# Performance work log

Measured on AMD Instinct MI355X. Metric: run time of the kernel, lower is better.

The kernel has to match this reference:

```python
import jax, jax.numpy as jnp
import numpy as np

EPS = 1e-6
INV_T = 100.0
STEPS = 7  # eval_steps


def setup_inputs() -> dict:
    key = jax.random.key(0)
    k1, k2 = jax.random.split(key)
    B, C, H, W, R = 8, 512, 128, 128, 64
    x = jax.random.uniform(k1, (B, C, H, W), dtype=jnp.float32)
    bases = jax.random.uniform(k2, (B, C, R), dtype=jnp.float32)
    # _build_bases: F.normalize(bases, dim=1) -> L2 normalize over D
    bases = bases / jnp.maximum(jnp.linalg.norm(bases, axis=1, keepdims=True), 1e-12)
    return {"x": x, "bases": bases}


def _nmf(xf, bases):
    # xf: [B, D, N], bases: [B, D, R]
    # coef init: softmax(inv_t * x^T @ bases) over R
    coef = jax.nn.softmax(INV_T * jnp.einsum('bdn,bdr->bnr', xf, bases), axis=-1)

    def step(carry, _):
        bases, coef = carry
        # multiplicative update for coef: coef * (x^T B) / (coef (B^T B))
        num = jnp.einsum('bdn,bdr->bnr', xf, bases)          # [B,N,R]
        den = coef @ (jnp.swapaxes(bases, 1, 2) @ bases)      # [B,N,R]
        coef = coef * num / (den + EPS)
        # multiplicative update for bases: B * (x coef) / (B (coef^T coef))
        num = jnp.einsum('bdn,bnr->bdr', xf, coef)            # [B,D,R]
        den = bases @ (jnp.swapaxes(coef, 1, 2) @ coef)       # [B,D,R]
        bases = bases * num / (den + EPS)
        return (bases, coef), None

    (bases, coef), _ = jax.lax.scan(step, (bases, coef), None, length=STEPS)
    # compute_coef: one final coef update
    num = jnp.einsum('bdn,bdr->bnr', xf, bases)
    den = coef @ (jnp.swapaxes(bases, 1, 2) @ bases)
    coef = coef * num / (den + EPS)
    return bases, coef


def reference(x, bases):
    B, C, H, W = x.shape
    N = H * W
    xf = x.reshape(B, C, N)  # S=1, D=C
    bases, coef = _nmf(xf, bases)
    out = jnp.einsum('bdr,bnr->bdn', bases, coef)  # bases @ coef^T
    return out.reshape(B, C, H, W)
```

## Files before the change

### kernel.cpp

```cpp
#include <hip/hip_runtime.h>
#include <cstdint>
#include <cstddef>

namespace {

constexpr int B_ = 8;
constexpr int D_ = 512;
constexpr int N_ = 16384;
constexpr int R_ = 64;
constexpr float EPS_ = 1e-6f;
constexpr float INVT_ = 100.0f;

typedef __attribute__((ext_vector_type(4))) float f32x4;
typedef __attribute__((ext_vector_type(8))) short s16x8;
typedef __attribute__((ext_vector_type(4))) short s16x4;

#define MFMA16(A, Bv, C) __builtin_amdgcn_mfma_f32_16x16x32_bf16(A, Bv, C, 0, 0, 0)

#define VMW(n) asm volatile("s_waitcnt vmcnt(" #n ")" ::: "memory")
#define LGKM0 asm volatile("s_waitcnt lgkmcnt(0)" ::: "memory")
#define SCHEDB __builtin_amdgcn_sched_barrier(0)
#define BARRIER do { SCHEDB; __builtin_amdgcn_s_barrier(); SCHEDB; } while (0)

typedef __attribute__((address_space(3))) unsigned int lds_u32_t;
typedef const __attribute__((address_space(1))) unsigned int glb_u32_t;

__device__ __forceinline__ void gl2lds16(const void* g, void* l) {
    __builtin_amdgcn_global_load_lds((glb_u32_t*)g, (lds_u32_t*)l, 16, 0, 0);
}

__device__ __forceinline__ unsigned short f2bf(float x) {
    unsigned int u = __float_as_uint(x);
    return (unsigned short)((u + 0x7fffu + ((u >> 16) & 1u)) >> 16);
}
__device__ __forceinline__ float bf2f(unsigned short u) {
    return __uint_as_float(((unsigned int)u) << 16);
}
__device__ __forceinline__ s16x8 ld8(const unsigned short* p) {
    return *reinterpret_cast<const s16x8*>(p);
}

__device__ __forceinline__ void stage16(const unsigned short* __restrict__ rowbase,
        size_t rstride_elems, unsigned short* __restrict__ buf, int w, int lane) {
#pragma unroll
    for (int i = 0; i < 4; ++i) {
        int r = w * 4 + i;
        const char* src = reinterpret_cast<const char*>(rowbase + (size_t)r * rstride_elems)
                        + ((lane << 4) ^ ((r & 7) << 4));
        gl2lds16(src, reinterpret_cast<char*>(buf) + r * 1024);
    }
}
__device__ __forceinline__ s16x8 read_t16(const unsigned short* buf, int row, int ks, int h4) {
    return *reinterpret_cast<const s16x8*>(reinterpret_cast<const char*>(buf)
        + row * 1024 + ((ks * 64 + h4 * 16) ^ ((row & 7) << 4)));
}
__device__ __forceinline__ void stage_c16(const unsigned short* __restrict__ cnr_n0,
        unsigned short* __restrict__ buf, int w, int lane) {
    int h = w & 1;
    int row = h * 8 + (lane >> 3);
    const char* src = reinterpret_cast<const char*>(cnr_n0 + (size_t)row * R_)
                    + ((((lane & 7) ^ (row & 7))) << 4);
    gl2lds16(src, reinterpret_cast<char*>(buf) + h * 1024);
}
__device__ __forceinline__ s16x8 read_c16(const unsigned short* buf, int row, int ks, int h4) {
    return *reinterpret_cast<const s16x8*>(reinterpret_cast<const char*>(buf)
        + row * 128 + ((ks * 64 + h4 * 16) ^ ((row & 7) << 4)));
}
__device__ __forceinline__ float read_c_scalar(const unsigned short* buf, int row, int r) {
    return bf2f(*reinterpret_cast<const unsigned short*>(
        reinterpret_cast<const char*>(buf) + row * 128 + ((r * 2) ^ ((row & 7) << 4))));
}

__global__ __launch_bounds__(256) void k_convert(const float* __restrict__ X,
        unsigned short* __restrict__ Xhi, unsigned short* __restrict__ XThi,
        unsigned short* __restrict__ XTlo, int have_lo) {
    __shared__ f32x4 lds4[64 * 16];
    int id = blockIdx.x;
    int nblk = id & 255, dblk = (id >> 8) & 7, b = id >> 11;
    int t = threadIdx.x;
    int d = t >> 2, c0 = (t & 3) * 16;
    const float* Xb = X + ((size_t)b * D_ + dblk * 64) * N_ + (size_t)nblk * 64;
    f32x4 v[4];
#pragma unroll
    for (int i = 0; i < 4; ++i)
        v[i] = *reinterpret_cast<const f32x4*>(Xb + (size_t)d * N_ + c0 + 4 * i);
    {
        int swz = (d ^ (d >> 3)) & 7;
#pragma unroll
        for (int i = 0; i < 4; ++i)
            lds4[d * 16 + ((((t & 3) << 2) + i) ^ swz)] = v[i];
    }
    {
        int dfull = dblk * 64 + d;
        int n0 = nblk * 64 + c0;
        unsigned short* dst = Xhi + (size_t)b * D_ * N_
                            + ((size_t)((dfull >> 4) * 32 + (n0 >> 9))) * 8192
                            + (dfull & 15) * 512 + (n0 & 511);
        s16x8 h0, h1;
#pragma unroll
        for (int k = 0; k < 8; ++k) {
            h0[k] = (short)f2bf(v[k >> 2][k & 3]);
            h1[k] = (short)f2bf(v[2 + (k >> 2)][k & 3]);
        }
        *reinterpret_cast<s16x8*>(dst) = h0;
        *reinterpret_cast<s16x8*>(dst + 8) = h1;
    }
    __syncthreads();
    {
        int n = t >> 2;
        const float* L = reinterpret_cast<const float*>(lds4);
        s16x8 h0, h1, l0, l1;
#pragma unroll
        for (int k = 0; k < 16; ++k) {
            int r = c0 + k;
            int sz = (r ^ (r >> 3)) & 7;
            float a = L[r * 64 + ((((n >> 2) ^ sz) << 2) | (n & 3))];
            unsigned short ha = f2bf(a);
            unsigned short la = f2bf(a - bf2f(ha));
            if (k < 8) { h0[k] = (short)ha; l0[k] = (short)la; }
            else       { h1[k - 8] = (short)ha; l1[k - 8] = (short)la; }
        }
        size_t off = ((size_t)b * N_ + nblk * 64 + n) * D_ + dblk * 64 + c0;
        *reinterpret_cast<s16x8*>(XThi + off) = h0;
        *reinterpret_cast<s16x8*>(XThi + off + 8) = h1;
        if (have_lo) {
            *reinterpret_cast<s16x8*>(XTlo + off) = l0;
            *reinterpret_cast<s16x8*>(XTlo + off + 8) = l1;
        }
    }
}

__global__ __launch_bounds__(256) void k_ginit(const float* __restrict__ Bin,
        float* __restrict__ bases, unsigned short* __restrict__ BThi,
        unsigned short* __restrict__ BTlo) {
    __shared__ float lds[64][65];
    int id = blockIdx.x, dblk = id & 7, b = id >> 3;
    int t = threadIdx.x, tn = t & 63, tq = t >> 6;
    const float* Bb = Bin + ((size_t)b * D_ + dblk * 64) * R_;
    float* bb = bases + ((size_t)b * D_ + dblk * 64) * R_;
#pragma unroll
    for (int i = 0; i < 16; ++i) {
        int d = i * 4 + tq;
        float v = Bb[d * R_ + tn];
        lds[d][tn] = v;
        bb[d * R_ + tn] = v;
    }
    __syncthreads();
#pragma unroll
    for (int i = 0; i < 16; ++i) {
        int r = i * 4 + tq;
        float v = lds[tn][r];
        unsigned short hi = f2bf(v);
        size_t off = ((size_t)b * R_ + r) * D_ + dblk * 64 + tn;
        BThi[off] = hi;
        BTlo[off] = f2bf(v - bf2f(hi));
    }
}

__global__ __launch_bounds__(256) void k_gram(const unsigned short* __restrict__ BT,
        unsigned short* __restrict__ G) {
    int b = blockIdx.x;
    int t = threadIdx.x, lane = t & 63, w = t >> 6;
    int m16 = lane & 15, h4 = lane >> 4;
    const unsigned short* BTb = BT + (size_t)b * R_ * D_;
    f32x4 acc[4];
#pragma unroll
    for (int j = 0; j < 4; ++j) acc[j] = (f32x4){0.f, 0.f, 0.f, 0.f};
#pragma unroll
    for (int k0 = 0; k0 < D_; k0 += 32) {
        int kg = k0 + (h4 << 3);
        s16x8 frag[4];
#pragma unroll
        for (int j = 0; j < 4; ++j)
            frag[j] = ld8(BTb + (size_t)(j * 16 + m16) * D_ + kg);
        s16x8 fw = ld8(BTb + (size_t)(w * 16 + m16) * D_ + kg);
#pragma unroll
        for (int j = 0; j < 4; ++j) acc[j] = MFMA16(fw, frag[j], acc[j]);
    }
    unsigned short* Gb = G + (size_t)b * R_ * R_;
#pragma unroll
    for (int j = 0; j < 4; ++j)
#pragma unroll
        for (int q = 0; q < 4; ++q) {
            int r1 = 16 * w + (h4 << 2) + q;
            Gb[r1 * R_ + 16 * j + m16] = f2bf(acc[j][q]);
        }
}

template <int LO>
__global__ __launch_bounds__(256, 2) void k_init(const unsigned short* __restrict__ XThi,
        const unsigned short* __restrict__ XTlo, const unsigned short* __restrict__ BThi,
        const unsigned short* __restrict__ BTlo, const unsigned short* __restrict__ G,
        unsigned short* __restrict__ CTb, unsigned short* __restrict__ Cnr) {
    __shared__ __align__(16) unsigned short xhbuf[2][16 * 512];
    __shared__ __align__(16) unsigned short xlbuf[LO ? 2 : 1][16 * 512];
    __shared__ __align__(16) unsigned short ldsc[16 * 64];
    __shared__ float red[2][4][16];
    int id = blockIdx.x, blk = id & 63, b = id >> 6;
    int t = threadIdx.x, lane = t & 63, w = t >> 6;
    int m16 = lane & 15, h4 = lane >> 4;
    const unsigned short* XTb = XThi + (size_t)b * N_ * D_;
    const unsigned short* XLb = XTlo + (size_t)b * N_ * D_;
    const unsigned short* BThb = BThi + (size_t)b * R_ * D_;
    const unsigned short* BTlb = BTlo + (size_t)b * R_ * D_;
    const unsigned short* Gb = G + (size_t)b * R_ * R_;
    unsigned short* CTbb = CTb + (size_t)b * R_ * N_;
    unsigned short* Cnrb = Cnr + (size_t)b * N_ * R_;
    s16x8 abh[16], abl[16], g[2];
#pragma unroll
    for (int ks = 0; ks < 16; ++ks) {
        size_t off = (size_t)(w * 16 + m16) * D_ + ks * 32 + h4 * 8;
        abh[ks] = ld8(BThb + off);
        abl[ks] = ld8(BTlb + off);
    }
#pragma unroll
    for (int ks = 0; ks < 2; ++ks)
        g[ks] = ld8(Gb + (size_t)(w * 16 + m16) * R_ + ks * 32 + h4 * 8);
    SCHEDB;
    stage16(XTb + (size_t)(blk * 16 + 0) * 16 * D_, D_, xhbuf[0], w, lane);
    if (LO) stage16(XLb + (size_t)(blk * 16 + 0) * 16 * D_, D_, xlbuf[0], w, lane);
    stage16(XTb + (size_t)(blk * 16 + 1) * 16 * D_, D_, xhbuf[1], w, lane);
    if (LO) stage16(XLb + (size_t)(blk * 16 + 1) * 16 * D_, D_, xlbuf[1], w, lane);
    SCHEDB;

    int swz = (m16 & 7) << 4;
    char* crow = reinterpret_cast<char*>(ldsc) + m16 * 128;

    for (int tt = 0; tt < 16; ++tt) {
        int cur = tt & 1;
        int n0 = (blk * 16 + tt) * 16;
        if (LO) {
            if (tt == 0) VMW(8);
            else if (tt == 15) VMW(5);
            else VMW(13);
        } else {
            if (tt == 0) VMW(4);
            else if (tt == 15) VMW(5);
            else VMW(9);
        }
        BARRIER;
        const unsigned short* xh = xhbuf[cur];
        const unsigned short* xl = xlbuf[LO ? cur : 0];
        f32x4 acc = (f32x4){0.f, 0.f, 0.f, 0.f};
#pragma unroll
        for (int ks = 0; ks < 16; ++ks) {
            s16x8 bh = read_t16(xh, m16, ks, h4);
            acc = MFMA16(abh[ks], bh, acc);
            acc = MFMA16(abl[ks], bh, acc);
            if (LO) {
                s16x8 bl = read_t16(xl, m16, ks, h4);
                acc = MFMA16(abh[ks], bl, acc);
            }
        }
        float mx = fmaxf(fmaxf(acc[0], acc[1]), fmaxf(acc[2], acc[3]));
        mx = fmaxf(mx, __shfl_xor(mx, 16));
        mx = fmaxf(mx, __shfl_xor(mx, 32));
        if (lane < 16) red[0][w][m16] = mx;
        LGKM0; BARRIER;
        mx = fmaxf(fmaxf(red[0][0][m16], red[0][1][m16]),
                   fmaxf(red[0][2][m16], red[0][3][m16]));
        float p[4], ss = 0.f;
#pragma unroll
        for (int q = 0; q < 4; ++q) {
            p[q] = __expf(INVT_ * (acc[q] - mx));
            ss += p[q];
        }
        ss += __shfl_xor(ss, 16);
        ss += __shfl_xor(ss, 32);
        if (lane < 16) red[1][w][m16] = ss;
        LGKM0; BARRIER;
        ss = red[1][0][m16] + red[1][1][m16] + red[1][2][m16] + red[1][3][m16];
        float inv = 1.f / ss;
#pragma unroll
        for (int q = 0; q < 4; ++q) {
            int r = w * 16 + h4 * 4 + q;
            *reinterpret_cast<unsigned short*>(crow + ((r * 2) ^ swz)) = f2bf(p[q] * inv);
        }
        LGKM0; BARRIER;
        f32x4 dacc = (f32x4){0.f, 0.f, 0.f, 0.f};
#pragma unroll
        for (int ks = 0; ks < 2; ++ks) {
            s16x8 bf = *reinterpret_cast<const s16x8*>(crow + ((ks * 64 + h4 * 16) ^ swz));
            dacc = MFMA16(g[ks], bf, dacc);
        }
        s16x4 cn;
        float c1v[4];
#pragma unroll
        for (int q = 0; q < 4; ++q) {
            c1v[q] = p[q] * inv * acc[q] / (dacc[q] + EPS_);
            cn[q] = (short)f2bf(c1v[q]);
        }
        LGKM0; BARRIER;
        SCHEDB;
#pragma unroll
        for (int q = 0; q < 4; ++q)
            CTbb[(size_t)(w * 16 + h4 * 4 + q) * N_ + n0 + m16] = f2bf(c1v[q]);
        *reinterpret_cast<s16x4*>(Cnrb + (size_t)(n0 + m16) * R_ + w * 16 + h4 * 4) = cn;
        SCHEDB;
        if (tt + 2 < 16) {
            stage16(XTb + (size_t)(blk * 16 + tt + 2) * 16 * D_, D_, xhbuf[cur], w, lane);
            if (LO) stage16(XLb + (size_t)(blk * 16 + tt + 2) * 16 * D_, D_, xlbuf[cur], w, lane);
        }
        SCHEDB;
    }
}

__global__ __launch_bounds__(256, 4) void k_cu(const unsigned short* __restrict__ XThi,
        const unsigned short* __restrict__ BThi, const unsigned short* __restrict__ G,
        unsigned short* __restrict__ CTb, unsigned short* __restrict__ Cnr) {
    __shared__ __align__(16) unsigned short xbuf[2][16 * 512];
    __shared__ __align__(16) unsigned short cbuf[2][16 * 64];
    int id = blockIdx.x, blk = id & 127, b = id >> 7;
    int t = threadIdx.x, lane = t & 63, w = t >> 6;
    int m16 = lane & 15, h4 = lane >> 4;
    const unsigned short* XTb = XThi + (size_t)b * N_ * D_;
    const unsigned short* BTb = BThi + (size_t)b * R_ * D_;
    const unsigned short* Gb = G + (size_t)b * R_ * R_;
    unsigned short* CTbb = CTb + (size_t)b * R_ * N_;
    unsigned short* Cnrb = Cnr + (size_t)b * N_ * R_;
    s16x8 abt[16], g[2];
#pragma unroll
    for (int ks = 0; ks < 16; ++ks)
        abt[ks] = ld8(BTb + (size_t)(w * 16 + m16) * D_ + ks * 32 + h4 * 8);
#pragma unroll
    for (int ks = 0; ks < 2; ++ks)
        g[ks] = ld8(Gb + (size_t)(w * 16 + m16) * R_ + ks * 32 + h4 * 8);
    SCHEDB;
    stage16(XTb + (size_t)(blk * 8 + 0) * 16 * D_, D_, xbuf[0], w, lane);
    stage_c16(Cnrb + (size_t)(blk * 8 + 0) * 16 * R_, cbuf[0], w, lane);
    stage16(XTb + (size_t)(blk * 8 + 1) * 16 * D_, D_, xbuf[1], w, lane);
    stage_c16(Cnrb + (size_t)(blk * 8 + 1) * 16 * R_, cbuf[1], w, lane);
    SCHEDB;

    for (int tt = 0; tt < 8; ++tt) {
        int cur = tt & 1;
        int n0 = (blk * 8 + tt) * 16;
        if (tt == 0) VMW(5);
        else if (tt == 7) VMW(5);
        else VMW(10);
        BARRIER;
        const unsigned short* xb = xbuf[cur];
        const unsigned short* cb = cbuf[cur];
        f32x4 acc = (f32x4){0.f, 0.f, 0.f, 0.f};
#pragma unroll
        for (int ks = 0; ks < 16; ++ks)
            acc = MFMA16(abt[ks], read_t16(xb, m16, ks, h4), acc);
        f32x4 dacc = (f32x4){0.f, 0.f, 0.f, 0.f};
#pragma unroll
        for (int ks = 0; ks < 2; ++ks)
            dacc = MFMA16(g[ks], read_c16(cb, m16, ks, h4), dacc);
        s16x4 cn;
        float c1v[4];
#pragma unroll
        for (int q = 0; q < 4; ++q) {
            int r = w * 16 + h4 * 4 + q;
            float cold = read_c_scalar(cb, m16, r);
            c1v[q] = cold * acc[q] / (dacc[q] + EPS_);
            cn[q] = (short)f2bf(c1v[q]);
        }
        LGKM0; BARRIER;
        SCHEDB;
#pragma unroll
        for (int q = 0; q < 4; ++q)
            CTbb[(size_t)(w * 16 + h4 * 4 + q) * N_ + n0 + m16] = f2bf(c1v[q]);
        *reinterpret_cast<s16x4*>(Cnrb + (size_t)(n0 + m16) * R_ + w * 16 + h4 * 4) = cn;
        SCHEDB;
        if (tt + 2 < 8) {
            stage16(XTb + (size_t)(blk * 8 + tt + 2) * 16 * D_, D_, xbuf[cur], w, lane);
            stage_c16(Cnrb + (size_t)(blk * 8 + tt + 2) * 16 * R_, cbuf[cur], w, lane);
        }
        SCHEDB;
    }
}

__global__ __launch_bounds__(256, 4) void k_bu1t(const unsigned short* __restrict__ Xhi,
        const unsigned short* __restrict__ CTb, unsigned short* __restrict__ wsN2,
        float* __restrict__ wsH) {
    __shared__ __align__(16) unsigned short xbuf[2][16 * 512];
    int id = blockIdx.x;
    int b = id >> 7, c = (id >> 2) & 31, dg = id & 3;
    int t = threadIdx.x, lane = t & 63, w = t >> 6;
    int m16 = lane & 15, h4 = lane >> 4;
    const unsigned short* Xb = Xhi + (size_t)b * D_ * N_;
    const unsigned short* Cbc = CTb + (size_t)b * R_ * N_ + c * 512;
    s16x8 act[16];
#pragma unroll
    for (int ks = 0; ks < 16; ++ks)
        act[ks] = ld8(Cbc + (size_t)(w * 16 + m16) * N_ + ks * 32 + h4 * 8);
    SCHEDB;
    stage16(Xb + ((size_t)((dg * 8 + 0) * 32 + c)) * 8192, 512, xbuf[0], w, lane);
    stage16(Xb + ((size_t)((dg * 8 + 1) * 32 + c)) * 8192, 512, xbuf[1], w, lane);
    SCHEDB;
    f32x4 hacc = (f32x4){0.f, 0.f, 0.f, 0.f};
    {
        const unsigned short* Hrow = Cbc + (size_t)(dg * 16 + m16) * N_;
#pragma unroll
        for (int gg = 0; gg < 4; ++gg) {
            SCHEDB;
            s16x8 hb[4];
#pragma unroll
            for (int j = 0; j < 4; ++j)
                hb[j] = ld8(Hrow + (gg * 4 + j) * 32 + h4 * 8);
#pragma unroll
            for (int j = 0; j < 4; ++j)
                hacc = MFMA16(act[gg * 4 + j], hb[j], hacc);
        }
    }
    SCHEDB;
    unsigned short* n2 = wsN2 + (size_t)(b * 32 + c) * R_ * D_;
    for (int tt = 0; tt < 8; ++tt) {
        int cur = tt & 1;
        int d0 = dg * 128 + tt * 16;
        if (tt == 0) VMW(4);
        else if (tt == 7) VMW(4);
        else VMW(8);
        BARRIER;
        const unsigned short* xb = xbuf[cur];
        f32x4 acc = (f32x4){0.f, 0.f, 0.f, 0.f};
#pragma unroll
        for (int ks = 0; ks < 16; ++ks)
            acc = MFMA16(act[ks], read_t16(xb, m16, ks, h4), acc);
        LGKM0; BARRIER;
        SCHEDB;
        if (tt + 2 < 8)
            stage16(Xb + ((size_t)((dg * 8 + tt + 2) * 32 + c)) * 8192, 512, xbuf[cur], w, lane);
        SCHEDB;
#pragma unroll
        for (int q = 0; q < 4; ++q)
            n2[(size_t)(w * 16 + h4 * 4 + q) * D_ + d0 + m16] = f2bf(acc[q]);
        SCHEDB;
    }
    float* Hp = wsH + (size_t)(b * 32 + c) * 4096;
#pragma unroll
    for (int q = 0; q < 4; ++q)
        Hp[(w * 16 + h4 * 4 + q) * R_ + dg * 16 + m16] = hacc[q];
}

__global__ __launch_bounds__(256) void k_hred(const float* __restrict__ wsH,
        float* __restrict__ Hf) {
    int id = blockIdx.x, q = id & 3, b = id >> 2;
    int t = threadIdx.x;
    int i = q * 1024 + t * 4;
    f32x4 s = (f32x4){0.f, 0.f, 0.f, 0.f};
    for (int c = 0; c < 32; ++c)
        s += *reinterpret_cast<const f32x4*>(wsH + ((size_t)b * 32 + c) * 4096 + i);
    *reinterpret_cast<f32x4*>(Hf + (size_t)b * 4096 + i) = s;
}

__global__ __launch_bounds__(256) void k_bu2(const unsigned short* __restrict__ wsN2,
        const float* __restrict__ Hf, float* __restrict__ bases,
        unsigned short* __restrict__ BThi, unsigned short* __restrict__ Bdr) {
    __shared__ float ldsH[64][64];
    __shared__ float ldsb[16][65];
    __shared__ float ldsn[16][65];
    int id = blockIdx.x, dblk = id & 31, b = id >> 5;
    int t = threadIdx.x;
    int d0 = dblk * 16;
    const float* Hb = Hf + (size_t)b * 4096;
#pragma unroll
    for (int i = 0; i < 4; ++i) {
        f32x4 v = *reinterpret_cast<const f32x4*>(Hb + i * 1024 + t * 4);
        *reinterpret_cast<f32x4*>(&ldsH[0][0] + i * 1024 + t * 4) = v;
    }
    {
        int d = t >> 4, p0 = (t & 15) * 4;
        f32x4 v = *reinterpret_cast<const f32x4*>(bases + ((size_t)b * D_ + d0 + d) * R_ + p0);
#pragma unroll
        for (int k = 0; k < 4; ++k) ldsb[d][p0 + k] = v[k];
    }
    __syncthreads();
#pragma unroll
    for (int j = 0; j < 4; ++j) {
        int i = t + 256 * j;
        int r = i >> 4, d = i & 15;
        float n2 = 0.f;
        for (int c = 0; c < 32; ++c)
            n2 += bf2f(wsN2[(((size_t)b * 32 + c) * R_ + r) * D_ + d0 + d]);
        float den = 0.f;
#pragma unroll 8
        for (int p = 0; p < 64; ++p) den += ldsb[d][p] * ldsH[p][r];
        ldsn[d][r] = ldsb[d][r] * n2 / (den + EPS_);
    }
    __syncthreads();
    {
        int d = t >> 4, r0 = (t & 15) * 4;
        f32x4 v;
        s16x4 hv;
#pragma unroll
        for (int k = 0; k < 4; ++k) {
            v[k] = ldsn[d][r0 + k];
            hv[k] = (short)f2bf(v[k]);
        }
        *reinterpret_cast<f32x4*>(bases + ((size_t)b * D_ + d0 + d) * R_ + r0) = v;
        *reinterpret_cast<s16x4*>((unsigned short*)Bdr + ((size_t)b * D_ + d0 + d) * R_ + r0) = hv;
    }
    {
        int r = t >> 2, dd = (t & 3) * 4;
        s16x4 hv;
#pragma unroll
        for (int k = 0; k < 4; ++k) hv[k] = (short)f2bf(ldsn[dd + k][r]);
        *reinterpret_cast<s16x4*>(BThi + ((size_t)b * R_ + r) * D_ + d0 + dd) = hv;
    }
}

__global__ __launch_bounds__(256, 2) void k_out(const unsigned short* __restrict__ Bdr,
        const unsigned short* __restrict__ Cnr, float* __restrict__ Out) {
    __shared__ float ldso[4][64 * 68 + 8];
    int id = blockIdx.x, nblk = id & 63, dblk = (id >> 6) & 7, b = id >> 9;
    int t = threadIdx.x, lane = t & 63, w = t >> 6;
    int m16 = lane & 15, h4 = lane >> 4;
    const unsigned short* Bb = Bdr + (size_t)b * D_ * R_;
    const unsigned short* Cb = Cnr + (size_t)b * N_ * R_;
    int d0 = dblk * 64, n0 = nblk * 256 + w * 64;
    f32x4 acc[4][4];
#pragma unroll
    for (int i = 0; i < 4; ++i)
#pragma unroll
        for (int j = 0; j < 4; ++j) acc[i][j] = (f32x4){0.f, 0.f, 0.f, 0.f};
#pragma unroll
    for (int k0 = 0; k0 < 64; k0 += 32) {
        int kg = k0 + (h4 << 3);
        s16x8 afrag[4], bfrag[4];
#pragma unroll
        for (int i = 0; i < 4; ++i)
            afrag[i] = ld8(Bb + (size_t)(d0 + i * 16 + m16) * R_ + kg);
#pragma unroll
        for (int j = 0; j < 4; ++j)
            bfrag[j] = ld8(Cb + (size_t)(n0 + j * 16 + m16) * R_ + kg);
#pragma unroll
        for (int i = 0; i < 4; ++i)
#pragma unroll
            for (int j = 0; j < 4; ++j)
                acc[i][j] = MFMA16(afrag[i], bfrag[j], acc[i][j]);
    }
#pragma unroll
    for (int i = 0; i < 4; ++i)
#pragma unroll
        for (int j = 0; j < 4; ++j)
#pragma unroll
            for (int q = 0; q < 4; ++q)
                ldso[w][(i * 16 + h4 * 4 + q) * 68 + j * 16 + m16] = acc[i][j][q];
    __syncthreads();
    float* Ob = Out + (size_t)b * D_ * N_ + (size_t)d0 * N_ + nblk * 256;
    int quad = lane >> 4, cc = (lane & 15) * 4;
#pragma unroll
    for (int i = 0; i < 16; ++i) {
        int d = w * 16 + i;
        f32x4 v = *reinterpret_cast<const f32x4*>(&ldso[quad][d * 68 + cc]);
        *reinterpret_cast<f32x4*>(Ob + (size_t)d * N_ + quad * 64 + cc) = v;
    }
}

}

extern "C" void kernel_launch(void* const* d_in, const int* in_sizes, int n_in,
                              void* d_out, int out_size, void* d_ws, size_t ws_size,
                              hipStream_t stream) {
    const float* X = (const float*)d_in[0];
    const float* Bin = (const float*)d_in[1];
    float* Out = (float*)d_out;
    char* ws = (char*)d_ws;

    const size_t o_Xhi  = 0;
    const size_t o_XThi = o_Xhi  + (size_t)B_ * D_ * N_ * 2;
    const size_t o_CTb  = o_XThi + (size_t)B_ * N_ * D_ * 2;
    const size_t o_Cnr  = o_CTb  + (size_t)B_ * R_ * N_ * 2;
    const size_t o_bas  = o_Cnr  + (size_t)B_ * N_ * R_ * 2;
    const size_t o_BThi = o_bas  + (size_t)B_ * D_ * R_ * 4;
    const size_t o_BTlo = o_BThi + (size_t)B_ * R_ * D_ * 2;
    const size_t o_Bdr  = o_BTlo + (size_t)B_ * R_ * D_ * 2;
    const size_t o_G    = o_Bdr  + (size_t)B_ * D_ * R_ * 2;
    const size_t o_H    = o_G    + (size_t)B_ * R_ * R_ * 2;
    const size_t o_Hf   = o_H    + (size_t)B_ * 32 * R_ * R_ * 4;
    const size_t o_N2   = o_Hf   + (size_t)B_ * R_ * R_ * 4;
    const size_t BASE   = o_N2   + (size_t)B_ * 32 * R_ * D_ * 2;
    const size_t o_XTlo = BASE;
    const size_t FULL   = o_XTlo + (size_t)B_ * N_ * D_ * 2;

    if (ws_size < BASE) return;
    int have_lo = ws_size >= FULL ? 1 : 0;

    unsigned short* Xhi  = (unsigned short*)(ws + o_Xhi);
    unsigned short* XThi = (unsigned short*)(ws + o_XThi);
    unsigned short* XTlo = (unsigned short*)(ws + (have_lo ? o_XTlo : o_XThi));
    unsigned short* CTb  = (unsigned short*)(ws + o_CTb);
    unsigned short* Cnr  = (unsigned short*)(ws + o_Cnr);
    float*          bas  = (float*)(ws + o_bas);
    unsigned short* BThi = (unsigned short*)(ws + o_BThi);
    unsigned short* BTlo = (unsigned short*)(ws + o_BTlo);
    unsigned short* Bdr  = (unsigned short*)(ws + o_Bdr);
    unsigned short* G    = (unsigned short*)(ws + o_G);
    float*          H    = (float*)(ws + o_H);
    float*          Hf   = (float*)(ws + o_Hf);
    unsigned short* N2   = (unsigned short*)(ws + o_N2);

    k_convert<<<dim3(16384), dim3(256), 0, stream>>>(X, Xhi, XThi, XTlo, have_lo);
    k_ginit<<<dim3(64), dim3(256), 0, stream>>>(Bin, bas, BThi, BTlo);
    k_gram<<<dim3(8), dim3(256), 0, stream>>>(BThi, G);
    if (have_lo)
        k_init<1><<<dim3(512), dim3(256), 0, stream>>>(XThi, XTlo, BThi, BTlo, G, CTb, Cnr);
    else
        k_init<0><<<dim3(512), dim3(256), 0, stream>>>(XThi, XTlo, BThi, BTlo, G, CTb, Cnr);
    for (int s = 0; s < 7; ++s) {
        k_bu1t<<<dim3(1024), dim3(256), 0, stream>>>(Xhi, CTb, N2, H);
        k_hred<<<dim3(32), dim3(256), 0, stream>>>(H, Hf);
        k_bu2<<<dim3(256), dim3(256), 0, stream>>>(N2, Hf, bas, BThi, Bdr);
        k_gram<<<dim3(8), dim3(256), 0, stream>>>(BThi, G);
        k_cu<<<dim3(1024), dim3(256), 0, stream>>>(XThi, BThi, G, CTb, Cnr);
    }
    k_out<<<dim3(4096), dim3(256), 0, stream>>>(Bdr, Cnr, Out);
}
```

Measured before the change: 1.195 ms.

## Replace H partial reduction kernel with atomics and enlarge convert tiles

```diff
diff --git a/kernel.cpp b/kernel.cpp
--- a/kernel.cpp
+++ b/kernel.cpp
@@ -74,58 +74,56 @@
 __global__ __launch_bounds__(256) void k_convert(const float* __restrict__ X,
         unsigned short* __restrict__ Xhi, unsigned short* __restrict__ XThi,
         unsigned short* __restrict__ XTlo, int have_lo) {
-    __shared__ f32x4 lds4[64 * 16];
+    __shared__ f32x4 lds4[128 * 32];
     int id = blockIdx.x;
-    int nblk = id & 255, dblk = (id >> 8) & 7, b = id >> 11;
+    int nblk = id & 127, dblk = (id >> 7) & 3, b = id >> 9;
     int t = threadIdx.x;
-    int d = t >> 2, c0 = (t & 3) * 16;
-    const float* Xb = X + ((size_t)b * D_ + dblk * 64) * N_ + (size_t)nblk * 64;
-    f32x4 v[4];
-#pragma unroll
-    for (int i = 0; i < 4; ++i)
-        v[i] = *reinterpret_cast<const f32x4*>(Xb + (size_t)d * N_ + c0 + 4 * i);
-    {
-        int swz = (d ^ (d >> 3)) & 7;
-#pragma unroll
-        for (int i = 0; i < 4; ++i)
-            lds4[d * 16 + ((((t & 3) << 2) + i) ^ swz)] = v[i];
-    }
-    {
-        int dfull = dblk * 64 + d;
-        int n0 = nblk * 64 + c0;
+    int d_loc = t >> 1, h = t & 1;
+    const float* Xb = X + ((size_t)b * D_ + dblk * 128) * N_ + (size_t)nblk * 128;
+    f32x4 v[16];
+#pragma unroll
+    for (int i = 0; i < 16; ++i)
+        v[i] = *reinterpret_cast<const f32x4*>(Xb + (size_t)d_loc * N_ + h * 64 + 4 * i);
+    {
+        int swz = (d_loc ^ (d_loc >> 3)) & 7;
+#pragma unroll
+        for (int i = 0; i < 16; ++i)
+            lds4[d_loc * 32 + ((h * 16 + i) ^ swz)] = v[i];
+    }
+    {
+        int dfull = dblk * 128 + d_loc;
+        int ngl = nblk * 128 + h * 64;
         unsigned short* dst = Xhi + (size_t)b * D_ * N_
-                            + ((size_t)((dfull >> 4) * 32 + (n0 >> 9))) * 8192
-                            + (dfull & 15) * 512 + (n0 & 511);
-        s16x8 h0, h1;
-#pragma unroll
-        for (int k = 0; k < 8; ++k) {
-            h0[k] = (short)f2bf(v[k >> 2][k & 3]);
-            h1[k] = (short)f2bf(v[2 + (k >> 2)][k & 3]);
-        }
-        *reinterpret_cast<s16x8*>(dst) = h0;
-        *reinterpret_cast<s16x8*>(dst + 8) = h1;
+                            + ((size_t)((dfull >> 4) * 32 + (ngl >> 9))) * 8192
+                            + (dfull & 15) * 512 + (ngl & 511);
+#pragma unroll
+        for (int i = 0; i < 8; ++i) {
+            s16x8 hv;
+#pragma unroll
+            for (int k = 0; k < 8; ++k)
+                hv[k] = (short)f2bf(v[i * 2 + (k >> 2)][k & 3]);
+            *reinterpret_cast<s16x8*>(dst + i * 8) = hv;
+        }
     }
     __syncthreads();
     {
-        int n = t >> 2;
+        int n_loc = t >> 1, hd = t & 1;
         const float* L = reinterpret_cast<const float*>(lds4);
-        s16x8 h0, h1, l0, l1;
-#pragma unroll
-        for (int k = 0; k < 16; ++k) {
-            int r = c0 + k;
-            int sz = (r ^ (r >> 3)) & 7;
-            float a = L[r * 64 + ((((n >> 2) ^ sz) << 2) | (n & 3))];
-            unsigned short ha = f2bf(a);
-            unsigned short la = f2bf(a - bf2f(ha));
-            if (k < 8) { h0[k] = (short)ha; l0[k] = (short)la; }
-            else       { h1[k - 8] = (short)ha; l1[k - 8] = (short)la; }
-        }
-        size_t off = ((size_t)b * N_ + nblk * 64 + n) * D_ + dblk * 64 + c0;
-        *reinterpret_cast<s16x8*>(XThi + off) = h0;
-        *reinterpret_cast<s16x8*>(XThi + off + 8) = h1;
-        if (have_lo) {
-            *reinterpret_cast<s16x8*>(XTlo + off) = l0;
-            *reinterpret_cast<s16x8*>(XTlo + off + 8) = l1;
+        size_t off = ((size_t)b * N_ + nblk * 128 + n_loc) * D_ + dblk * 128 + hd * 64;
+#pragma unroll
+        for (int i = 0; i < 8; ++i) {
+            s16x8 hv, lv;
+#pragma unroll
+            for (int k = 0; k < 8; ++k) {
+                int dl = hd * 64 + i * 8 + k;
+                int swz = (dl ^ (dl >> 3)) & 7;
+                float a = L[dl * 128 + ((((n_loc >> 2) ^ swz) << 2) | (n_loc & 3))];
+                unsigned short ha = f2bf(a);
+                hv[k] = (short)ha;
+                lv[k] = (short)f2bf(a - bf2f(ha));
+            }
+            *reinterpret_cast<s16x8*>(XThi + off + i * 8) = hv;
+            if (have_lo) *reinterpret_cast<s16x8*>(XTlo + off + i * 8) = lv;
         }
     }
 }
@@ -158,10 +156,16 @@
 }
 
 __global__ __launch_bounds__(256) void k_gram(const unsigned short* __restrict__ BT,
-        unsigned short* __restrict__ G) {
+        unsigned short* __restrict__ G, float* __restrict__ Hf, int zf) {
     int b = blockIdx.x;
     int t = threadIdx.x, lane = t & 63, w = t >> 6;
     int m16 = lane & 15, h4 = lane >> 4;
+    if (zf) {
+        float* Hz = Hf + (size_t)b * 4096;
+#pragma unroll
+        for (int i = 0; i < 4; ++i)
+            *reinterpret_cast<f32x4*>(Hz + i * 1024 + t * 4) = (f32x4){0.f, 0.f, 0.f, 0.f};
+    }
     const unsigned short* BTb = BT + (size_t)b * R_ * D_;
     f32x4 acc[4];
 #pragma unroll
@@ -375,7 +379,7 @@
 
 __global__ __launch_bounds__(256, 4) void k_bu1t(const unsigned short* __restrict__ Xhi,
         const unsigned short* __restrict__ CTb, unsigned short* __restrict__ wsN2,
-        float* __restrict__ wsH) {
+        float* __restrict__ Hf, int sp) {
     __shared__ __align__(16) unsigned short xbuf[2][16 * 512];
     int id = blockIdx.x;
     int b = id >> 7, c = (id >> 2) & 31, dg = id & 3;
@@ -430,25 +434,14 @@
             n2[(size_t)(w * 16 + h4 * 4 + q) * D_ + d0 + m16] = f2bf(acc[q]);
         SCHEDB;
     }
-    float* Hp = wsH + (size_t)(b * 32 + c) * 4096;
+    float* Hfb = Hf + (size_t)sp * (B_ * 4096) + (size_t)b * 4096;
 #pragma unroll
     for (int q = 0; q < 4; ++q)
-        Hp[(w * 16 + h4 * 4 + q) * R_ + dg * 16 + m16] = hacc[q];
-}
-
-__global__ __launch_bounds__(256) void k_hred(const float* __restrict__ wsH,
-        float* __restrict__ Hf) {
-    int id = blockIdx.x, q = id & 3, b = id >> 2;
-    int t = threadIdx.x;
-    int i = q * 1024 + t * 4;
-    f32x4 s = (f32x4){0.f, 0.f, 0.f, 0.f};
-    for (int c = 0; c < 32; ++c)
-        s += *reinterpret_cast<const f32x4*>(wsH + ((size_t)b * 32 + c) * 4096 + i);
-    *reinterpret_cast<f32x4*>(Hf + (size_t)b * 4096 + i) = s;
+        atomicAdd(&Hfb[(w * 16 + h4 * 4 + q) * R_ + dg * 16 + m16], hacc[q]);
 }
 
 __global__ __launch_bounds__(256) void k_bu2(const unsigned short* __restrict__ wsN2,
-        const float* __restrict__ Hf, float* __restrict__ bases,
+        float* __restrict__ Hf, int sp, float* __restrict__ bases,
         unsigned short* __restrict__ BThi, unsigned short* __restrict__ Bdr) {
     __shared__ float ldsH[64][64];
     __shared__ float ldsb[16][65];
@@ -456,7 +449,11 @@
     int id = blockIdx.x, dblk = id & 31, b = id >> 5;
     int t = threadIdx.x;
     int d0 = dblk * 16;
-    const float* Hb = Hf + (size_t)b * 4096;
+    {
+        float* Hz = Hf + (size_t)(1 - sp) * (B_ * 4096) + (size_t)id * 128;
+        if (t < 32) *reinterpret_cast<f32x4*>(Hz + t * 4) = (f32x4){0.f, 0.f, 0.f, 0.f};
+    }
+    const float* Hb = Hf + (size_t)sp * (B_ * 4096) + (size_t)b * 4096;
 #pragma unroll
     for (int i = 0; i < 4; ++i) {
         f32x4 v = *reinterpret_cast<const f32x4*>(Hb + i * 1024 + t * 4);
@@ -570,9 +567,8 @@
     const size_t o_BTlo = o_BThi + (size_t)B_ * R_ * D_ * 2;
     const size_t o_Bdr  = o_BTlo + (size_t)B_ * R_ * D_ * 2;
     const size_t o_G    = o_Bdr  + (size_t)B_ * D_ * R_ * 2;
-    const size_t o_H    = o_G    + (size_t)B_ * R_ * R_ * 2;
-    const size_t o_Hf   = o_H    + (size_t)B_ * 32 * R_ * R_ * 4;
-    const size_t o_N2   = o_Hf   + (size_t)B_ * R_ * R_ * 4;
+    const size_t o_Hf   = o_G    + (size_t)B_ * R_ * R_ * 2;
+    const size_t o_N2   = o_Hf   + (size_t)2 * B_ * R_ * R_ * 4;
     const size_t BASE   = o_N2   + (size_t)B_ * 32 * R_ * D_ * 2;
     const size_t o_XTlo = BASE;
     const size_t FULL   = o_XTlo + (size_t)B_ * N_ * D_ * 2;
@@ -590,22 +586,21 @@
     unsigned short* BTlo = (unsigned short*)(ws + o_BTlo);
     unsigned short* Bdr  = (unsigned short*)(ws + o_Bdr);
     unsigned short* G    = (unsigned short*)(ws + o_G);
-    float*          H    = (float*)(ws + o_H);
     float*          Hf   = (float*)(ws + o_Hf);
     unsigned short* N2   = (unsigned short*)(ws + o_N2);
 
-    k_convert<<<dim3(16384), dim3(256), 0, stream>>>(X, Xhi, XThi, XTlo, have_lo);
+    k_convert<<<dim3(4096), dim3(256), 0, stream>>>(X, Xhi, XThi, XTlo, have_lo);
     k_ginit<<<dim3(64), dim3(256), 0, stream>>>(Bin, bas, BThi, BTlo);
-    k_gram<<<dim3(8), dim3(256), 0, stream>>>(BThi, G);
+    k_gram<<<dim3(8), dim3(256), 0, stream>>>(BThi, G, Hf, 1);
     if (have_lo)
         k_init<1><<<dim3(512), dim3(256), 0, stream>>>(XThi, XTlo, BThi, BTlo, G, CTb, Cnr);
     else
         k_init<0><<<dim3(512), dim3(256), 0, stream>>>(XThi, XTlo, BThi, BTlo, G, CTb, Cnr);
     for (int s = 0; s < 7; ++s) {
-        k_bu1t<<<dim3(1024), dim3(256), 0, stream>>>(Xhi, CTb, N2, H);
-        k_hred<<<dim3(32), dim3(256), 0, stream>>>(H, Hf);
-        k_bu2<<<dim3(256), dim3(256), 0, stream>>>(N2, Hf, bas, BThi, Bdr);
-        k_gram<<<dim3(8), dim3(256), 0, stream>>>(BThi, G);
+        int sp = s & 1;
+        k_bu1t<<<dim3(1024), dim3(256), 0, stream>>>(Xhi, CTb, N2, Hf, sp);
+        k_bu2<<<dim3(256), dim3(256), 0, stream>>>(N2, Hf, sp, bas, BThi, Bdr);
+        k_gram<<<dim3(8), dim3(256), 0, stream>>>(BThi, G, Hf, 0);
         k_cu<<<dim3(1024), dim3(256), 0, stream>>>(XThi, BThi, G, CTb, Cnr);
     }
     k_out<<<dim3(4096), dim3(256), 0, stream>>>(Bdr, Cnr, Out);
```

Measured after the change: 1.244 ms. 4.0% more time.
